# Kernel optimization log

Hardware: AMD Instinct MI355X
Metric: run time of the kernel (lower is better)

The kernel has to match this reference:

```python
import jax, jax.numpy as jnp
import numpy as np

# H2RConfig constants
KERNEL = 3
MAX_ROUTES = 1000
STRIDE = 4.0
MIN_SIZE = 32.0
MAX_SIZE = 512.0
SCORE_POWER = 2.0
UNC_WEIGHT = 0.35


def setup_inputs() -> dict:
    key = jax.random.key(0)
    k1, k2, k3 = jax.random.split(key, 3)
    shape = (32, 1, 512, 512)  # [B, 1, H, W] heatmaps at stride 4
    return {
        "route_logits": jax.random.normal(k1, shape, jnp.float32),
        "scale_logits": jax.random.normal(k2, shape, jnp.float32),
        "uncertainty_logits": jax.random.normal(k3, shape, jnp.float32),
        "image_h": 2048,
        "image_w": 2048,
    }


def reference(route_logits, scale_logits, uncertainty_logits, image_h, image_w):
    # score map: sigmoid^power, modulated by uncertainty (use_route_uncertainty=True)
    score = jnp.power(jax.nn.sigmoid(route_logits), SCORE_POWER)
    score = score * (1.0 - UNC_WEIGHT * jax.nn.sigmoid(uncertainty_logits))

    # local-max NMS: 3x3 max pool, stride 1, SAME padding (torch pads with -inf)
    pooled = jax.lax.reduce_window(
        score, -jnp.inf, jax.lax.max,
        window_dimensions=(1, 1, KERNEL, KERNEL),
        window_strides=(1, 1, 1, 1),
        padding="SAME",
    )
    peak_mask = score == pooled
    filtered = jnp.where(peak_mask, score, -1.0)

    B = score.shape[0]
    Wd = score.shape[3]
    flat = filtered.reshape(B, -1)                 # [B, H*W]
    values, indices = jax.lax.top_k(flat, MAX_ROUTES)  # [B, K]
    valid = values > 0.0                            # torch drops these; we mask/pad

    ys = indices // Wd
    xs = indices % Wd
    cx = (xs.astype(jnp.float32) + 0.5) * STRIDE
    cy = (ys.astype(jnp.float32) + 0.5) * STRIDE

    # gather scale / uncertainty at peak locations
    sc = jnp.take_along_axis(scale_logits.reshape(B, -1), indices, axis=1)
    un = jax.nn.sigmoid(jnp.take_along_axis(uncertainty_logits.reshape(B, -1), indices, axis=1))

    side = MIN_SIZE + jax.nn.sigmoid(sc) * (MAX_SIZE - MIN_SIZE)
    side = side * (1.0 + 0.25 * un)
    half = side * 0.5

    iw = float(image_w)
    ih = float(image_h)
    x1 = jnp.clip(cx - half, 0.0, iw - 1.0)
    y1 = jnp.clip(cy - half, 0.0, ih - 1.0)
    x2 = jnp.clip(cx + half, 1.0, iw)
    y2 = jnp.clip(cy + half, 1.0, ih)

    bcol = jnp.broadcast_to(jnp.arange(B, dtype=jnp.float32)[:, None], values.shape)
    rois = jnp.stack([bcol, x1, y1, x2, y2], axis=-1)  # [B, K, 5]

    # padded (fixed-shape) equivalent of torch's variable-length concat
    rois = jnp.where(valid[..., None], rois, 0.0)
    scores = jnp.where(valid, values, 0.0)
    return rois, scores, valid
```

## Files before the change

### kernel.cpp

```cpp
#include <hip/hip_runtime.h>
#include <hip/hip_bf16.h>
#include <math.h>


#define B_   32
#define H_   512
#define W_   512
#define HW_  (H_ * W_)
#define K_   1000
#define ROWS_ 16
#define THR_  512
#define NSTRIP_ 32
#define NBUK_ 4096
#define GCAP_ 2048
#define HOTCAP_ 896
#define HOTPAIR_ (NSTRIP_ * HOTCAP_ / 2)
#define HOTBITS_ 0x3F000000u
#define WBASE_ (NBUK_ - 64)
#define FBCAP_ 45056

#define HL_BYTES_  ((size_t)B_ * NSTRIP_ * HOTCAP_ * 8)
#define GW_BYTES_  ((size_t)B_ * NSTRIP_ * 64 * 4)
#define FB_BYTES_  ((size_t)B_ * FBCAP_ * 8)

__device__ __forceinline__ float np_expf(float x) {
#pragma clang fp contract(off)
    const float log2e = 1.44269504088896341f;
    float z = x * log2e;
    float m = rintf(z);
    float r = fmaf(m, -0.693359375f, x);
    r = fmaf(m, 2.12194440e-4f, r);
    float r2 = r * r;
    float p = fmaf(1.9875691500e-4f, r, 1.3981999507e-3f);
    p = fmaf(p, r, 8.3334519073e-3f);
    p = fmaf(p, r, 4.1665795894e-2f);
    p = fmaf(p, r, 1.6666665459e-1f);
    p = fmaf(p, r, 5.0000001201e-1f);
    p = fmaf(p, r2, r);
    p = p + 1.0f;
    int mi = (int)m;
    float sc = __int_as_float((127 + mi) << 23);
    return p * sc;
}

__device__ __forceinline__ float sigmoid_np(float x) {
#pragma clang fp contract(off)
    float e = np_expf(-x);
    float d = 1.0f + e;
    return 1.0f / d;
}

__device__ __forceinline__ float score_ref(float r, float u) {
#pragma clang fp contract(off)
    float s  = sigmoid_np(r);
    float s2 = s * s;
    float su = sigmoid_np(u);
    float t  = 0.35f * su;
    float m  = 1.0f - t;
    return s2 * m;
}

__device__ __forceinline__ float sigmoid_fast(float x) {
    return 1.0f / (1.0f + __expf(-x));
}

__global__ __launch_bounds__(THR_, 4) void fused_peak_kernel(
    const float* __restrict__ route, const float* __restrict__ unc,
    unsigned long long* __restrict__ hotlist,
    unsigned int* __restrict__ ghw)
{
    __shared__ float sm[ROWS_ + 2][W_];
    __shared__ unsigned int whist[64];
    __shared__ int hcnt;

    const int tid   = threadIdx.x;
    const int lane  = tid & 63;
    const int strip = blockIdx.x;
    const int b     = blockIdx.y;
    const int r0    = strip * ROWS_;
    if (tid < 64) whist[tid] = 0u;
    if (tid == 0) hcnt = 0;

    const float4* rb4 = (const float4*)(route + (size_t)b * HW_);
    const float4* ub4 = (const float4*)(unc   + (size_t)b * HW_);
    unsigned long long* hseg =
        hotlist + (size_t)(b * NSTRIP_ + strip) * HOTCAP_;

    float4 rv[5], uv[5];
    int lrow[5], c4[5]; bool ok[5];
    #pragma unroll
    for (int k = 0; k < 5; ++k) {
        int slot = tid + k * THR_;
        slot = slot < 2303 ? slot : 2303;
        int row = slot >> 7;
        int gy  = r0 - 1 + row;
        lrow[k] = row; c4[k] = slot & 127;
        ok[k]   = (gy >= 0 && gy < H_);
        int cy  = gy < 0 ? 0 : (gy >= H_ ? H_ - 1 : gy);
        rv[k] = rb4[cy * 128 + c4[k]];
        uv[k] = ub4[cy * 128 + c4[k]];
    }
    #pragma unroll
    for (int k = 0; k < 5; ++k) {
        float4 s;
        s.x = score_ref(rv[k].x, uv[k].x);
        s.y = score_ref(rv[k].y, uv[k].y);
        s.z = score_ref(rv[k].z, uv[k].z);
        s.w = score_ref(rv[k].w, uv[k].w);
        if (!ok[k]) { s.x = -INFINITY; s.y = -INFINITY;
                      s.z = -INFINITY; s.w = -INFINITY; }
        *(float4*)&sm[lrow[k]][c4[k] * 4] = s;
    }
    __syncthreads();

    const unsigned long long lt = (1ull << lane) - 1ull;
    #pragma unroll
    for (int j = 0; j < 4; ++j) {
        int g  = tid + j * THR_;
        int ly = 1 + (g >> 7);
        int x0 = (g & 127) * 4;
        int gy = r0 + (ly - 1);
        float4 q0 = *(const float4*)&sm[ly - 1][x0];
        float4 q1 = *(const float4*)&sm[ly    ][x0];
        float4 q2 = *(const float4*)&sm[ly + 1][x0];
        bool hasL = (x0 > 0), hasR = (x0 + 4 < W_);
        float l0 = hasL ? sm[ly - 1][x0 - 1] : -INFINITY;
        float l1 = hasL ? sm[ly    ][x0 - 1] : -INFINITY;
        float l2 = hasL ? sm[ly + 1][x0 - 1] : -INFINITY;
        float e0 = hasR ? sm[ly - 1][x0 + 4] : -INFINITY;
        float e1 = hasR ? sm[ly    ][x0 + 4] : -INFINITY;
        float e2 = hasR ? sm[ly + 1][x0 + 4] : -INFINITY;
        float f_m1 = fmaxf(l0, fmaxf(l1, l2));
        float f_0  = fmaxf(q0.x, fmaxf(q1.x, q2.x));
        float f_1  = fmaxf(q0.y, fmaxf(q1.y, q2.y));
        float f_2  = fmaxf(q0.z, fmaxf(q1.z, q2.z));
        float f_3  = fmaxf(q0.w, fmaxf(q1.w, q2.w));
        float f_4  = fmaxf(e0, fmaxf(e1, e2));
        float tb0  = fmaxf(q0.x, q2.x);
        float tb1  = fmaxf(q0.y, q2.y);
        float tb2  = fmaxf(q0.z, q2.z);
        float tb3  = fmaxf(q0.w, q2.w);
        float vv[4] = { q1.x, q1.y, q1.z, q1.w };
        float mm[4];
        mm[0] = fmaxf(fmaxf(f_m1, f_1), tb0);
        mm[1] = fmaxf(fmaxf(f_0,  f_2), tb1);
        mm[2] = fmaxf(fmaxf(f_1,  f_3), tb2);
        mm[3] = fmaxf(fmaxf(f_2,  f_4), tb3);
        #pragma unroll
        for (int i = 0; i < 4; ++i) {
            bool take = (vv[i] >= mm[i]);
            unsigned int bits = __float_as_uint(vv[i]);
            bool hot = take && (bits >= HOTBITS_);
            unsigned long long hmk = __ballot(hot);
            if (hmk) {
                int ldr = __ffsll(hmk) - 1;
                int hb = 0;
                if (lane == ldr) hb = atomicAdd(&hcnt, __popcll(hmk));
                hb = __shfl(hb, ldr, 64);
                if (hot) {
                    int hp = hb + __popcll(hmk & lt);
                    if (hp < HOTCAP_) {
                        unsigned int idx = (unsigned int)(gy * W_ + x0 + i);
                        hseg[hp] = ((unsigned long long)bits << 32)
                                   | (0xFFFFFFFFu - idx);
                        atomicAdd(&whist[(bits >> 18) - WBASE_], 1u);
                    }
                }
            }
        }
    }
    __syncthreads();

    {
        int hn = hcnt < HOTCAP_ ? hcnt : HOTCAP_;
        for (int i = hn + tid; i < HOTCAP_; i += THR_) hseg[i] = 0ull;
    }
    if (tid < 64)
        ghw[(size_t)(b * NSTRIP_ + strip) * 64 + tid] = whist[tid];
}

__global__ __launch_bounds__(1024) void select2_kernel(
    const float* __restrict__ route, const float* __restrict__ unc_r,
    const float* __restrict__ scale, const float* __restrict__ unc,
    const unsigned long long* __restrict__ hotlist,
    const unsigned int* __restrict__ ghw,
    unsigned long long* __restrict__ fbbuf,
    const int* __restrict__ ih_p, const int* __restrict__ iw_p,
    float* __restrict__ out)
{
    __shared__ __align__(16) unsigned char u_[(ROWS_ + 2) * W_ * 4];
    __shared__ unsigned int hist[NBUK_];
    __shared__ int sh_T, sh_nc, sh_fb, sh_fn;

    float (*sm)[W_] = (float (*)[W_])u_;
    unsigned int* cursor = (unsigned int*)u_;
    unsigned long long* grp = (unsigned long long*)(u_ + 16384);

    const int b = blockIdx.x, tid = threadIdx.x;
    const int lane = tid & 63, wid = tid >> 6;

    if (tid == 0) { sh_fb = 0; sh_T = 1; sh_nc = 0; sh_fn = 0; }
    if (tid < 64) hist[WBASE_ + tid] = 0u;
    __syncthreads();
    {
        const unsigned int* gw = ghw + (size_t)b * NSTRIP_ * 64;
        for (int i = tid; i < NSTRIP_ * 64; i += 1024) {
            unsigned int v = gw[i];
            if (v) atomicAdd(&hist[WBASE_ + (i & 63)], v);
        }
    }
    __syncthreads();

    if (wid == 0) {
        int cnt = (int)hist[WBASE_ + lane];
        int sum = cnt;
        #pragma unroll
        for (int off = 32; off > 0; off >>= 1)
            sum += __shfl_down(sum, off, 64);
        sum = __shfl(sum, 0, 64);
        if (sum < K_) {
            if (lane == 0) sh_fb = 1;
        } else {
            int suf = cnt;
            #pragma unroll
            for (int off = 1; off < 64; off <<= 1) {
                int o = __shfl_down(suf, off, 64);
                suf += (lane + off < 64) ? o : 0;
            }
            bool cond = suf >= K_;
            unsigned long long mask = __ballot(cond);
            int ls = 63 - __builtin_clzll(mask);
            if (lane >= ls) cursor[WBASE_ + lane] = (unsigned int)(suf - cnt);
            int ncv = __shfl(suf, ls, 64);
            if (lane == 0) { sh_T = WBASE_ + ls; sh_nc = ncv; }
        }
    }
    __syncthreads();
    const int fb = sh_fb;

    if (fb) {
        for (int i = tid; i < NBUK_; i += 1024) hist[i] = 0u;
        __syncthreads();

        const float4* rb4 = (const float4*)(route + (size_t)b * HW_);
        const float4* ub4 = (const float4*)(unc_r + (size_t)b * HW_);
        unsigned long long* fbb = fbbuf + (size_t)b * FBCAP_;

        for (int strip = 0; strip < NSTRIP_; ++strip) {
            const int r0 = strip * ROWS_;
            __syncthreads();
            for (int slot = tid; slot < 2304; slot += 1024) {
                int row = slot >> 7;
                int gy  = r0 - 1 + row;
                int c4  = slot & 127;
                bool okr = (gy >= 0 && gy < H_);
                int cy  = gy < 0 ? 0 : (gy >= H_ - 1 ? H_ - 1 : gy);
                float4 r4 = rb4[cy * 128 + c4];
                float4 u4 = ub4[cy * 128 + c4];
                float4 s;
                s.x = score_ref(r4.x, u4.x);
                s.y = score_ref(r4.y, u4.y);
                s.z = score_ref(r4.z, u4.z);
                s.w = score_ref(r4.w, u4.w);
                if (!okr) { s.x = -INFINITY; s.y = -INFINITY;
                            s.z = -INFINITY; s.w = -INFINITY; }
                *(float4*)&sm[row][c4 * 4] = s;
            }
            __syncthreads();
            for (int g = tid; g < 4 * 512; g += 1024) {
                int ly = 1 + (g >> 7);
                (void)ly;
            }
            for (int g = tid; g < 2048; g += 1024) {
                int ly = 1 + (g >> 7);
                int x0 = (g & 127) * 4;
                int gy = r0 + (ly - 1);
                float4 q0 = *(const float4*)&sm[ly - 1][x0];
                float4 q1 = *(const float4*)&sm[ly    ][x0];
                float4 q2 = *(const float4*)&sm[ly + 1][x0];
                bool hasL = (x0 > 0), hasR = (x0 + 4 < W_);
                float l0 = hasL ? sm[ly - 1][x0 - 1] : -INFINITY;
                float l1 = hasL ? sm[ly    ][x0 - 1] : -INFINITY;
                float l2 = hasL ? sm[ly + 1][x0 - 1] : -INFINITY;
                float e0 = hasR ? sm[ly - 1][x0 + 4] : -INFINITY;
                float e1 = hasR ? sm[ly    ][x0 + 4] : -INFINITY;
                float e2 = hasR ? sm[ly + 1][x0 + 4] : -INFINITY;
                float f_m1 = fmaxf(l0, fmaxf(l1, l2));
                float f_0  = fmaxf(q0.x, fmaxf(q1.x, q2.x));
                float f_1  = fmaxf(q0.y, fmaxf(q1.y, q2.y));
                float f_2  = fmaxf(q0.z, fmaxf(q1.z, q2.z));
                float f_3  = fmaxf(q0.w, fmaxf(q1.w, q2.w));
                float f_4  = fmaxf(e0, fmaxf(e1, e2));
                float tb0  = fmaxf(q0.x, q2.x);
                float tb1  = fmaxf(q0.y, q2.y);
                float tb2  = fmaxf(q0.z, q2.z);
                float tb3  = fmaxf(q0.w, q2.w);
                float vv[4] = { q1.x, q1.y, q1.z, q1.w };
                float mm[4];
                mm[0] = fmaxf(fmaxf(f_m1, f_1), tb0);
                mm[1] = fmaxf(fmaxf(f_0,  f_2), tb1);
                mm[2] = fmaxf(fmaxf(f_1,  f_3), tb2);
                mm[3] = fmaxf(fmaxf(f_2,  f_4), tb3);
                #pragma unroll
                for (int i = 0; i < 4; ++i) {
                    if (vv[i] >= mm[i]) {
                        unsigned int bits = __float_as_uint(vv[i]);
                        unsigned int idx  = (unsigned int)(gy * W_ + x0 + i);
                        int p = atomicAdd(&sh_fn, 1);
                        if (p < FBCAP_) {
                            fbb[p] = ((unsigned long long)bits << 32)
                                     | (0xFFFFFFFFu - idx);
                            atomicAdd(&hist[bits >> 18], 1u);
                        }
                    }
                }
            }
        }
        __syncthreads();

        if (wid == 0) {
            int Tv = 0;
            int total = 0;
            for (int c = NBUK_ / 64 - 1; c >= 0; --c) {
                int cnt = (int)hist[c * 64 + lane];
                int sum = cnt;
                #pragma unroll
                for (int off = 32; off > 0; off >>= 1)
                    sum += __shfl_down(sum, off, 64);
                sum = __shfl(sum, 0, 64);
                if (total + sum < K_) { total += sum; continue; }
                int suf = cnt;
                #pragma unroll
                for (int off = 1; off < 64; off <<= 1) {
                    int o = __shfl_down(suf, off, 64);
                    suf += (lane + off < 64) ? o : 0;
                }
                bool cond = (total + suf) >= K_;
                unsigned long long mask = __ballot(cond);
                int ls = 63 - __builtin_clzll(mask);
                Tv = c * 64 + ls;
                break;
            }
            if (Tv < 1) Tv = 1;
            int run = 0;
            for (int cb = NBUK_ - 64; cb >= (Tv & ~63); cb -= 64) {
                int beta = cb + lane;
                int cnt = (beta >= Tv) ? (int)hist[beta] : 0;
                int suf = cnt;
                #pragma unroll
                for (int off = 1; off < 64; off <<= 1) {
                    int o = __shfl_down(suf, off, 64);
                    suf += (lane + off < 64) ? o : 0;
                }
                int chunk_total = __shfl(suf, 0, 64);
                if (beta >= Tv) cursor[beta] = (unsigned int)(run + (suf - cnt));
                run += chunk_total;
            }
            if (lane == 0) { sh_T = Tv; sh_nc = run; }
        }
    }
    __syncthreads();
    const unsigned int T = (unsigned int)sh_T;

    if (!fb) {
        const ulonglong2* src =
            (const ulonglong2*)(hotlist + (size_t)b * NSTRIP_ * HOTCAP_);
        for (int i = tid; i < HOTPAIR_; i += 1024) {
            ulonglong2 a = src[i];
            unsigned int b0 = (unsigned int)(a.x >> 50);
            unsigned int b1 = (unsigned int)(a.y >> 50);
            if (b0 >= T) {
                unsigned int pos = atomicAdd(&cursor[b0], 1u);
                if (pos < GCAP_) grp[pos] = a.x;
            }
            if (b1 >= T) {
                unsigned int pos = atomicAdd(&cursor[b1], 1u);
                if (pos < GCAP_) grp[pos] = a.y;
            }
        }
    } else {
        const unsigned long long* fbb = fbbuf + (size_t)b * FBCAP_;
        int n = sh_fn; if (n > FBCAP_) n = FBCAP_;
        for (int i = tid; i < n; i += 1024) {
            unsigned long long k = fbb[i];
            unsigned int b0 = (unsigned int)(k >> 50);
            if (b0 >= T) {
                unsigned int pos = atomicAdd(&cursor[b0], 1u);
                if (pos < GCAP_) grp[pos] = k;
            }
        }
    }
    __syncthreads();

    const float fih = (float)(*ih_p);
    const float fiw = (float)(*iw_p);
    float* rois   = out;
    float* scores = out + (size_t)B_ * K_ * 5;
    float* validf = out + (size_t)B_ * K_ * 6;

    int nc = sh_nc;
    int ncEff = nc < GCAP_ ? nc : GCAP_;
    for (int p = tid; p < ncEff; p += 1024) {
        unsigned long long key = grp[p];
        unsigned int beta = (unsigned int)(key >> 50);
        int segEnd   = (int)cursor[beta];
        int segStart = segEnd - (int)hist[beta];
        int qEnd = segEnd < GCAP_ ? segEnd : GCAP_;
        int r = 0;
        for (int q = segStart; q < qEnd; ++q)
            r += (grp[q] > key) ? 1 : 0;
        int rank = segStart + r;
        if (rank < K_) {
            int o = b * K_ + rank;
            unsigned int bits = (unsigned int)(key >> 32);
            float v = __uint_as_float(bits);
            unsigned int idx = 0xFFFFFFFFu - (unsigned int)(key & 0xFFFFFFFFull);
            int y = (int)(idx >> 9), x = (int)(idx & 511u);
            float cx = ((float)x + 0.5f) * 4.0f;
            float cy = ((float)y + 0.5f) * 4.0f;
            float ss = sigmoid_fast(scale[(size_t)b * HW_ + idx]);
            float su = sigmoid_fast(unc  [(size_t)b * HW_ + idx]);
            float side = (32.0f + ss * 480.0f) * (1.0f + 0.25f * su);
            float half = 0.5f * side;
            float x1 = fminf(fmaxf(cx - half, 0.0f), fiw - 1.0f);
            float y1 = fminf(fmaxf(cy - half, 0.0f), fih - 1.0f);
            float x2 = fminf(fmaxf(cx + half, 1.0f), fiw);
            float y2 = fminf(fmaxf(cy + half, 1.0f), fih);
            rois[o * 5 + 0] = (float)b;
            rois[o * 5 + 1] = x1; rois[o * 5 + 2] = y1;
            rois[o * 5 + 3] = x2; rois[o * 5 + 4] = y2;
            scores[o] = v; validf[o] = 1.0f;
        }
    }
    for (int k = nc + tid; k < K_; k += 1024) {
        int o = b * K_ + k;
        rois[o * 5 + 0] = 0.0f; rois[o * 5 + 1] = 0.0f;
        rois[o * 5 + 2] = 0.0f; rois[o * 5 + 3] = 0.0f;
        rois[o * 5 + 4] = 0.0f;
        scores[o] = 0.0f; validf[o] = 0.0f;
    }
}

extern "C" void kernel_launch(void* const* d_in, const int* in_sizes, int n_in,
                              void* d_out, int out_size, void* d_ws, size_t ws_size,
                              hipStream_t stream) {
    const float* route = (const float*)d_in[0];
    const float* scale = (const float*)d_in[1];
    const float* unc   = (const float*)d_in[2];
    const int*   ih    = (const int*)d_in[3];
    const int*   iw    = (const int*)d_in[4];
    float* out = (float*)d_out;

    unsigned char* base = (unsigned char*)d_ws;
    unsigned long long* hotlist = (unsigned long long*)base;
    unsigned int* ghw = (unsigned int*)(base + HL_BYTES_);
    unsigned long long* fbbuf =
        (unsigned long long*)(base + HL_BYTES_ + GW_BYTES_);

    dim3 g(NSTRIP_, B_);
    fused_peak_kernel<<<g, THR_, 0, stream>>>(route, unc, hotlist, ghw);
    select2_kernel<<<B_, 1024, 0, stream>>>(route, unc, scale, unc,
                                            hotlist, ghw, fbbuf,
                                            ih, iw, out);
}
```

Baseline: 158.6 us.

## Fuse peak and select kernels with last-strip-block spin-wait on per-wave done flags

Merges the two launches into one kernel. Each wave writes its own fixed-capacity hot segment with no shared counter atomics, then publishes a checksummed done record. The last strip block of each batch spins until all 256 segment records validate, then runs the threshold, candidate compaction and a full O(n^2) rank. This removes a launch and the per-block zero-fill of the hot lists. The risks are a deadlock if the last-strip blocks are scheduled before their producers, correctness that depends on stale done words from earlier calls not forming a valid checksum, and a quadratic rank over up to 2048 candidates.

```diff
diff --git a/kernel.cpp b/kernel.cpp
--- a/kernel.cpp
+++ b/kernel.cpp
@@ -12,16 +12,20 @@
 #define THR_  512
 #define NSTRIP_ 32
 #define NBUK_ 4096
-#define GCAP_ 2048
-#define HOTCAP_ 896
-#define HOTPAIR_ (NSTRIP_ * HOTCAP_ / 2)
+#define CAND_ 2048
+#define HSEG_ 112
+#define NSEGB_ (NSTRIP_ * 8)
 #define HOTBITS_ 0x3F000000u
 #define WBASE_ (NBUK_ - 64)
 #define FBCAP_ 45056
 
-#define HL_BYTES_  ((size_t)B_ * NSTRIP_ * HOTCAP_ * 8)
+#define C1_ 0x13579BDFu
+#define C2_ 0xECA86420u
+
+#define HL_BYTES_  ((size_t)B_ * NSEGB_ * HSEG_ * 8)
 #define GW_BYTES_  ((size_t)B_ * NSTRIP_ * 64 * 4)
-#define FB_BYTES_  ((size_t)B_ * FBCAP_ * 8)
+#define DN_BYTES_  ((size_t)B_ * NSEGB_ * 16)
+#define GF_BYTES_  ((size_t)B_ * NBUK_ * 4)
 
 __device__ __forceinline__ float np_expf(float x) {
 #pragma clang fp contract(off)
@@ -64,56 +68,83 @@
     return 1.0f / (1.0f + __expf(-x));
 }
 
-__global__ __launch_bounds__(THR_, 4) void fused_peak_kernel(
+__device__ __forceinline__ bool seg_done(const unsigned int* dw, int seg,
+                                         unsigned int* cnt) {
+    unsigned int w0 = __hip_atomic_load(dw + seg * 4 + 0, __ATOMIC_ACQUIRE,
+                                        __HIP_MEMORY_SCOPE_AGENT);
+    unsigned int w1 = __hip_atomic_load(dw + seg * 4 + 1, __ATOMIC_RELAXED,
+                                        __HIP_MEMORY_SCOPE_AGENT);
+    unsigned int w2 = __hip_atomic_load(dw + seg * 4 + 2, __ATOMIC_RELAXED,
+                                        __HIP_MEMORY_SCOPE_AGENT);
+    unsigned int w3 = __hip_atomic_load(dw + seg * 4 + 3, __ATOMIC_RELAXED,
+                                        __HIP_MEMORY_SCOPE_AGENT);
+    *cnt = w0;
+    return (w1 == ~w0) && (w2 == (w0 ^ C1_)) && (w3 == (w0 ^ C2_));
+}
+
+__global__ __launch_bounds__(THR_, 8) void h2r_kernel(
     const float* __restrict__ route, const float* __restrict__ unc,
+    const float* __restrict__ scale,
     unsigned long long* __restrict__ hotlist,
-    unsigned int* __restrict__ ghw)
+    unsigned int* __restrict__ ghw,
+    unsigned int* __restrict__ done_,
+    unsigned int* __restrict__ ghfb,
+    unsigned long long* __restrict__ fbbuf,
+    const int* __restrict__ ih_p, const int* __restrict__ iw_p,
+    float* __restrict__ out)
 {
-    __shared__ float sm[ROWS_ + 2][W_];
+    __shared__ __align__(16) unsigned char smb[(ROWS_ + 2) * W_ * 4];
     __shared__ unsigned int whist[64];
-    __shared__ int hcnt;
+    __shared__ unsigned int wsum[64];
+    __shared__ int segc[NSEGB_];
+    __shared__ int sh_T, sh_nc, sh_fb, sh_n, sh_fn;
+
+    float (*sm)[W_] = (float (*)[W_])smb;
 
     const int tid   = threadIdx.x;
     const int lane  = tid & 63;
+    const int wid   = tid >> 6;
     const int strip = blockIdx.x;
     const int b     = blockIdx.y;
     const int r0    = strip * ROWS_;
     if (tid < 64) whist[tid] = 0u;
-    if (tid == 0) hcnt = 0;
 
     const float4* rb4 = (const float4*)(route + (size_t)b * HW_);
     const float4* ub4 = (const float4*)(unc   + (size_t)b * HW_);
     unsigned long long* hseg =
-        hotlist + (size_t)(b * NSTRIP_ + strip) * HOTCAP_;
-
-    float4 rv[5], uv[5];
-    int lrow[5], c4[5]; bool ok[5];
-    #pragma unroll
-    for (int k = 0; k < 5; ++k) {
-        int slot = tid + k * THR_;
-        slot = slot < 2303 ? slot : 2303;
-        int row = slot >> 7;
-        int gy  = r0 - 1 + row;
-        lrow[k] = row; c4[k] = slot & 127;
-        ok[k]   = (gy >= 0 && gy < H_);
-        int cy  = gy < 0 ? 0 : (gy >= H_ ? H_ - 1 : gy);
-        rv[k] = rb4[cy * 128 + c4[k]];
-        uv[k] = ub4[cy * 128 + c4[k]];
-    }
-    #pragma unroll
-    for (int k = 0; k < 5; ++k) {
-        float4 s;
-        s.x = score_ref(rv[k].x, uv[k].x);
-        s.y = score_ref(rv[k].y, uv[k].y);
-        s.z = score_ref(rv[k].z, uv[k].z);
-        s.w = score_ref(rv[k].w, uv[k].w);
-        if (!ok[k]) { s.x = -INFINITY; s.y = -INFINITY;
-                      s.z = -INFINITY; s.w = -INFINITY; }
-        *(float4*)&sm[lrow[k]][c4[k] * 4] = s;
+        hotlist + ((size_t)b * NSEGB_ + strip * 8 + wid) * HSEG_;
+
+    {
+        float4 rv[5], uv[5];
+        int lrow[5], c4[5]; bool ok[5];
+        #pragma unroll
+        for (int k = 0; k < 5; ++k) {
+            int slot = tid + k * THR_;
+            slot = slot < 2303 ? slot : 2303;
+            int row = slot >> 7;
+            int gy  = r0 - 1 + row;
+            lrow[k] = row; c4[k] = slot & 127;
+            ok[k]   = (gy >= 0 && gy < H_);
+            int cy  = gy < 0 ? 0 : (gy >= H_ ? H_ - 1 : gy);
+            rv[k] = rb4[cy * 128 + c4[k]];
+            uv[k] = ub4[cy * 128 + c4[k]];
+        }
+        #pragma unroll
+        for (int k = 0; k < 5; ++k) {
+            float4 s;
+            s.x = score_ref(rv[k].x, uv[k].x);
+            s.y = score_ref(rv[k].y, uv[k].y);
+            s.z = score_ref(rv[k].z, uv[k].z);
+            s.w = score_ref(rv[k].w, uv[k].w);
+            if (!ok[k]) { s.x = -INFINITY; s.y = -INFINITY;
+                          s.z = -INFINITY; s.w = -INFINITY; }
+            *(float4*)&sm[lrow[k]][c4[k] * 4] = s;
+        }
     }
     __syncthreads();
 
     const unsigned long long lt = (1ull << lane) - 1ull;
+    int wn = 0;
     #pragma unroll
     for (int j = 0; j < 4; ++j) {
         int g  = tid + j * THR_;
@@ -152,67 +183,68 @@
             unsigned int bits = __float_as_uint(vv[i]);
             bool hot = take && (bits >= HOTBITS_);
             unsigned long long hmk = __ballot(hot);
-            if (hmk) {
-                int ldr = __ffsll(hmk) - 1;
-                int hb = 0;
-                if (lane == ldr) hb = atomicAdd(&hcnt, __popcll(hmk));
-                hb = __shfl(hb, ldr, 64);
-                if (hot) {
-                    int hp = hb + __popcll(hmk & lt);
-                    if (hp < HOTCAP_) {
-                        unsigned int idx = (unsigned int)(gy * W_ + x0 + i);
-                        hseg[hp] = ((unsigned long long)bits << 32)
-                                   | (0xFFFFFFFFu - idx);
-                        atomicAdd(&whist[(bits >> 18) - WBASE_], 1u);
-                    }
-                }
-            }
-        }
-    }
-    __syncthreads();
-
-    {
-        int hn = hcnt < HOTCAP_ ? hcnt : HOTCAP_;
-        for (int i = hn + tid; i < HOTCAP_; i += THR_) hseg[i] = 0ull;
-    }
+            if (hot) {
+                int hp = wn + __popcll(hmk & lt);
+                if (hp < HSEG_) {
+                    unsigned int idx = (unsigned int)(gy * W_ + x0 + i);
+                    hseg[hp] = ((unsigned long long)bits << 32)
+                               | (0xFFFFFFFFu - idx);
+                    atomicAdd(&whist[(bits >> 18) - WBASE_], 1u);
+                }
+            }
+            wn += __popcll(hmk);
+        }
+    }
+    __syncthreads();
+
     if (tid < 64)
         ghw[(size_t)(b * NSTRIP_ + strip) * 64 + tid] = whist[tid];
-}
-
-__global__ __launch_bounds__(1024) void select2_kernel(
-    const float* __restrict__ route, const float* __restrict__ unc_r,
-    const float* __restrict__ scale, const float* __restrict__ unc,
-    const unsigned long long* __restrict__ hotlist,
-    const unsigned int* __restrict__ ghw,
-    unsigned long long* __restrict__ fbbuf,
-    const int* __restrict__ ih_p, const int* __restrict__ iw_p,
-    float* __restrict__ out)
-{
-    __shared__ __align__(16) unsigned char u_[(ROWS_ + 2) * W_ * 4];
-    __shared__ unsigned int hist[NBUK_];
-    __shared__ int sh_T, sh_nc, sh_fb, sh_fn;
-
-    float (*sm)[W_] = (float (*)[W_])u_;
-    unsigned int* cursor = (unsigned int*)u_;
-    unsigned long long* grp = (unsigned long long*)(u_ + 16384);
-
-    const int b = blockIdx.x, tid = threadIdx.x;
-    const int lane = tid & 63, wid = tid >> 6;
-
-    if (tid == 0) { sh_fb = 0; sh_T = 1; sh_nc = 0; sh_fn = 0; }
-    if (tid < 64) hist[WBASE_ + tid] = 0u;
-    __syncthreads();
+    {
+        int stored = wn < HSEG_ ? wn : HSEG_;
+        if (lane == 0) {
+            unsigned int v = (unsigned int)stored;
+            unsigned int* d = done_ + ((size_t)b * NSEGB_ + strip * 8 + wid) * 4;
+            __hip_atomic_store(d + 1, ~v,     __ATOMIC_RELAXED, __HIP_MEMORY_SCOPE_AGENT);
+            __hip_atomic_store(d + 2, v ^ C1_, __ATOMIC_RELAXED, __HIP_MEMORY_SCOPE_AGENT);
+            __hip_atomic_store(d + 3, v ^ C2_, __ATOMIC_RELAXED, __HIP_MEMORY_SCOPE_AGENT);
+            __hip_atomic_store(d + 0, v,      __ATOMIC_RELEASE, __HIP_MEMORY_SCOPE_AGENT);
+        }
+    }
+
+    if (strip != NSTRIP_ - 1) return;
+
+    if (tid == 0) { sh_fb = 0; sh_T = 1; sh_nc = 0; sh_n = 0; sh_fn = 0; }
+    if (tid < 64) wsum[tid] = 0u;
+
+    if (wid == 0) {
+        const unsigned int* dw = done_ + (size_t)b * NSEGB_ * 4;
+        unsigned int c0, c1, c2, c3;
+        for (;;) {
+            bool ok = seg_done(dw, lane,       &c0);
+            ok &= seg_done(dw, lane + 64,  &c1);
+            ok &= seg_done(dw, lane + 128, &c2);
+            ok &= seg_done(dw, lane + 192, &c3);
+            if (__all(ok)) break;
+            __builtin_amdgcn_s_sleep(1);
+        }
+        segc[lane]       = (int)c0;
+        segc[lane + 64]  = (int)c1;
+        segc[lane + 128] = (int)c2;
+        segc[lane + 192] = (int)c3;
+    }
+    __syncthreads();
+
     {
         const unsigned int* gw = ghw + (size_t)b * NSTRIP_ * 64;
-        for (int i = tid; i < NSTRIP_ * 64; i += 1024) {
+        for (int i = tid; i < NSTRIP_ * 64; i += THR_) {
             unsigned int v = gw[i];
-            if (v) atomicAdd(&hist[WBASE_ + (i & 63)], v);
+            if (v) atomicAdd(&wsum[i & 63], v);
         }
     }
     __syncthreads();
 
     if (wid == 0) {
-        int cnt = (int)hist[WBASE_ + lane];
+        int cnt = (int)wsum[lane];
         int sum = cnt;
         #pragma unroll
         for (int off = 32; off > 0; off >>= 1)
@@ -230,51 +262,73 @@
             bool cond = suf >= K_;
             unsigned long long mask = __ballot(cond);
             int ls = 63 - __builtin_clzll(mask);
-            if (lane >= ls) cursor[WBASE_ + lane] = (unsigned int)(suf - cnt);
             int ncv = __shfl(suf, ls, 64);
             if (lane == 0) { sh_T = WBASE_ + ls; sh_nc = ncv; }
         }
     }
     __syncthreads();
     const int fb = sh_fb;
-
-    if (fb) {
-        for (int i = tid; i < NBUK_; i += 1024) hist[i] = 0u;
+    unsigned long long* cand = (unsigned long long*)smb;
+
+    if (!fb) {
+        const unsigned int T = (unsigned int)sh_T;
+        for (int s = wid; s < NSEGB_; s += 8) {
+            int c = segc[s];
+            const unsigned long long* hs =
+                hotlist + ((size_t)b * NSEGB_ + s) * HSEG_;
+            for (int base = 0; base < c; base += 64) {
+                int i = base + lane;
+                bool act = (i < c);
+                unsigned long long key = act ? hs[i] : 0ull;
+                bool take = act && ((unsigned int)(key >> 50) >= T);
+                unsigned long long mk = __ballot(take);
+                if (mk) {
+                    int ldr = __ffsll(mk) - 1;
+                    int bp = 0;
+                    if (lane == ldr) bp = atomicAdd(&sh_n, __popcll(mk));
+                    bp = __shfl(bp, ldr, 64);
+                    if (take) {
+                        int p = bp + __popcll(mk & lt);
+                        if (p < CAND_) cand[p] = key;
+                    }
+                }
+            }
+        }
+    } else {
+        unsigned int* gh = ghfb + (size_t)b * NBUK_;
+        unsigned long long* fbb = fbbuf + (size_t)b * FBCAP_;
+        for (int i = tid; i < NBUK_; i += THR_) gh[i] = 0u;
         __syncthreads();
 
-        const float4* rb4 = (const float4*)(route + (size_t)b * HW_);
-        const float4* ub4 = (const float4*)(unc_r + (size_t)b * HW_);
-        unsigned long long* fbb = fbbuf + (size_t)b * FBCAP_;
-
-        for (int strip = 0; strip < NSTRIP_; ++strip) {
-            const int r0 = strip * ROWS_;
+        for (int st = 0; st < NSTRIP_; ++st) {
+            const int rr = st * ROWS_;
             __syncthreads();
-            for (int slot = tid; slot < 2304; slot += 1024) {
-                int row = slot >> 7;
-                int gy  = r0 - 1 + row;
-                int c4  = slot & 127;
-                bool okr = (gy >= 0 && gy < H_);
-                int cy  = gy < 0 ? 0 : (gy >= H_ - 1 ? H_ - 1 : gy);
-                float4 r4 = rb4[cy * 128 + c4];
-                float4 u4 = ub4[cy * 128 + c4];
-                float4 s;
-                s.x = score_ref(r4.x, u4.x);
-                s.y = score_ref(r4.y, u4.y);
-                s.z = score_ref(r4.z, u4.z);
-                s.w = score_ref(r4.w, u4.w);
-                if (!okr) { s.x = -INFINITY; s.y = -INFINITY;
-                            s.z = -INFINITY; s.w = -INFINITY; }
-                *(float4*)&sm[row][c4 * 4] = s;
+            for (int slot0 = 0; slot0 < 2304; slot0 += THR_) {
+                int slot = slot0 + tid;
+                if (slot < 2304) {
+                    int row = slot >> 7;
+                    int gy  = rr - 1 + row;
+                    int c4  = slot & 127;
+                    bool okr = (gy >= 0 && gy < H_);
+                    int cy  = gy < 0 ? 0 : (gy >= H_ ? H_ - 1 : gy);
+                    float4 r4 = rb4[cy * 128 + c4];
+                    float4 u4 = ub4[cy * 128 + c4];
+                    float4 s;
+                    s.x = score_ref(r4.x, u4.x);
+                    s.y = score_ref(r4.y, u4.y);
+                    s.z = score_ref(r4.z, u4.z);
+                    s.w = score_ref(r4.w, u4.w);
+                    if (!okr) { s.x = -INFINITY; s.y = -INFINITY;
+                                s.z = -INFINITY; s.w = -INFINITY; }
+                    *(float4*)&sm[row][c4 * 4] = s;
+                }
             }
             __syncthreads();
-            for (int g = tid; g < 4 * 512; g += 1024) {
-                int ly = 1 + (g >> 7);
-                (void)ly;
-            }
-            for (int g = tid; g < 2048; g += 1024) {
+            for (int g0 = 0; g0 < 2048; g0 += THR_) {
+                int g  = g0 + tid;
                 int ly = 1 + (g >> 7);
                 int x0 = (g & 127) * 4;
-                int gy = r0 + (ly - 1);
+                int gy = rr + (ly - 1);
                 float4 q0 = *(const float4*)&sm[ly - 1][x0];
                 float4 q1 = *(const float4*)&sm[ly    ][x0];
                 float4 q2 = *(const float4*)&sm[ly + 1][x0];
@@ -310,7 +364,7 @@
                         if (p < FBCAP_) {
                             fbb[p] = ((unsigned long long)bits << 32)
                                      | (0xFFFFFFFFu - idx);
-                            atomicAdd(&hist[bits >> 18], 1u);
+                            atomicAdd(&gh[bits >> 18], 1u);
                         }
                     }
                 }
@@ -319,10 +373,9 @@
         __syncthreads();
 
         if (wid == 0) {
-            int Tv = 0;
-            int total = 0;
+            int Tv = 1, ncv = 0, total = 0;
             for (int c = NBUK_ / 64 - 1; c >= 0; --c) {
-                int cnt = (int)hist[c * 64 + lane];
+                int cnt = (int)gh[c * 64 + lane];
                 int sum = cnt;
                 #pragma unroll
                 for (int off = 32; off > 0; off >>= 1)
@@ -339,54 +392,30 @@
                 unsigned long long mask = __ballot(cond);
                 int ls = 63 - __builtin_clzll(mask);
                 Tv = c * 64 + ls;
+                ncv = total + __shfl(suf, ls, 64);
                 break;
             }
             if (Tv < 1) Tv = 1;
-            int run = 0;
-            for (int cb = NBUK_ - 64; cb >= (Tv & ~63); cb -= 64) {
-                int beta = cb + lane;
-                int cnt = (beta >= Tv) ? (int)hist[beta] : 0;
-                int suf = cnt;
-                #pragma unroll
-                for (int off = 1; off < 64; off <<= 1) {
-                    int o = __shfl_down(suf, off, 64);
-                    suf += (lane + off < 64) ? o : 0;
-                }
-                int chunk_total = __shfl(suf, 0, 64);
-                if (beta >= Tv) cursor[beta] = (unsigned int)(run + (suf - cnt));
-                run += chunk_total;
-            }
-            if (lane == 0) { sh_T = Tv; sh_nc = run; }
-        }
-    }
-    __syncthreads();
-    const unsigned int T = (unsigned int)sh_T;
-
-    if (!fb) {
-        const ulonglong2* src =
-            (const ulonglong2*)(hotlist + (size_t)b * NSTRIP_ * HOTCAP_);
-        for (int i = tid; i < HOTPAIR_; i += 1024) {
-            ulonglong2 a = src[i];
-            unsigned int b0 = (unsigned int)(a.x >> 50);
-            unsigned int b1 = (unsigned int)(a.y >> 50);
-            if (b0 >= T) {
-                unsigned int pos = atomicAdd(&cursor[b0], 1u);
-                if (pos < GCAP_) grp[pos] = a.x;
-            }
-            if (b1 >= T) {
-                unsigned int pos = atomicAdd(&cursor[b1], 1u);
-                if (pos < GCAP_) grp[pos] = a.y;
-            }
-        }
-    } else {
-        const unsigned long long* fbb = fbbuf + (size_t)b * FBCAP_;
+            if (lane == 0) { sh_T = Tv; sh_nc = ncv; }
+        }
+        __syncthreads();
+        const unsigned int T = (unsigned int)sh_T;
         int n = sh_fn; if (n > FBCAP_) n = FBCAP_;
-        for (int i = tid; i < n; i += 1024) {
-            unsigned long long k = fbb[i];
-            unsigned int b0 = (unsigned int)(k >> 50);
-            if (b0 >= T) {
-                unsigned int pos = atomicAdd(&cursor[b0], 1u);
-                if (pos < GCAP_) grp[pos] = k;
+        for (int i0 = 0; i0 < n; i0 += THR_) {
+            int i = i0 + tid;
+            bool act = (i < n);
+            unsigned long long key = act ? fbb[i] : 0ull;
+            bool take = act && ((unsigned int)(key >> 50) >= T);
+            unsigned long long mk = __ballot(take);
+            if (mk) {
+                int ldr = __ffsll(mk) - 1;
+                int bp = 0;
+                if (lane == ldr) bp = atomicAdd(&sh_n, __popcll(mk));
+                bp = __shfl(bp, ldr, 64);
+                if (take) {
+                    int p = bp + __popcll(mk & lt);
+                    if (p < CAND_) cand[p] = key;
+                }
             }
         }
     }
@@ -398,20 +427,14 @@
     float* scores = out + (size_t)B_ * K_ * 5;
     float* validf = out + (size_t)B_ * K_ * 6;
 
-    int nc = sh_nc;
-    int ncEff = nc < GCAP_ ? nc : GCAP_;
-    for (int p = tid; p < ncEff; p += 1024) {
-        unsigned long long key = grp[p];
-        unsigned int beta = (unsigned int)(key >> 50);
-        int segEnd   = (int)cursor[beta];
-        int segStart = segEnd - (int)hist[beta];
-        int qEnd = segEnd < GCAP_ ? segEnd : GCAP_;
+    int ncA = sh_n; if (ncA > CAND_) ncA = CAND_;
+    for (int p = tid; p < ncA; p += THR_) {
+        unsigned long long key = cand[p];
         int r = 0;
-        for (int q = segStart; q < qEnd; ++q)
-            r += (grp[q] > key) ? 1 : 0;
-        int rank = segStart + r;
-        if (rank < K_) {
-            int o = b * K_ + rank;
+        for (int q = 0; q < ncA; ++q)
+            r += (cand[q] > key) ? 1 : 0;
+        if (r < K_) {
+            int o = b * K_ + r;
             unsigned int bits = (unsigned int)(key >> 32);
             float v = __uint_as_float(bits);
             unsigned int idx = 0xFFFFFFFFu - (unsigned int)(key & 0xFFFFFFFFull);
@@ -432,7 +455,7 @@
             scores[o] = v; validf[o] = 1.0f;
         }
     }
-    for (int k = nc + tid; k < K_; k += 1024) {
+    for (int k = sh_nc + tid; k < K_; k += THR_) {
         int o = b * K_ + k;
         rois[o * 5 + 0] = 0.0f; rois[o * 5 + 1] = 0.0f;
         rois[o * 5 + 2] = 0.0f; rois[o * 5 + 3] = 0.0f;
@@ -453,13 +476,13 @@
 
     unsigned char* base = (unsigned char*)d_ws;
     unsigned long long* hotlist = (unsigned long long*)base;
-    unsigned int* ghw = (unsigned int*)(base + HL_BYTES_);
+    unsigned int* ghw  = (unsigned int*)(base + HL_BYTES_);
+    unsigned int* done_ = (unsigned int*)(base + HL_BYTES_ + GW_BYTES_);
+    unsigned int* ghfb = (unsigned int*)(base + HL_BYTES_ + GW_BYTES_ + DN_BYTES_);
     unsigned long long* fbbuf =
-        (unsigned long long*)(base + HL_BYTES_ + GW_BYTES_);
+        (unsigned long long*)(base + HL_BYTES_ + GW_BYTES_ + DN_BYTES_ + GF_BYTES_);
 
     dim3 g(NSTRIP_, B_);
-    fused_peak_kernel<<<g, THR_, 0, stream>>>(route, unc, hotlist, ghw);
-    select2_kernel<<<B_, 1024, 0, stream>>>(route, unc, scale, unc,
-                                            hotlist, ghw, fbbuf,
-                                            ih, iw, out);
-}
+    h2r_kernel<<<g, THR_, 0, stream>>>(route, unc, scale, hotlist, ghw,
+                                       done_, ghfb, fbbuf, ih, iw, out);
+}
```

New measurement: 375.4 us. +136.8%, slower.
